# Kernel optimization log

Hardware: AMD Instinct MI355X
Metric: run time of the kernel (lower is better)

## Reference

```python
import jax, jax.numpy as jnp
import numpy as np

N = 100000      # nodes
E = 3200000     # edges (avg degree 32)
F_IN = 512      # input features
H = 16          # hidden (module default)
C = 40          # classes


def _linear_params(key, fan_in, fan_out):
    # torch.nn.Linear default init: U(-1/sqrt(fan_in), 1/sqrt(fan_in))
    k1, k2 = jax.random.split(key)
    lim = 1.0 / np.sqrt(fan_in)
    W = jax.random.uniform(k1, (fan_in, fan_out), jnp.float32, -lim, lim)
    b = jax.random.uniform(k2, (fan_out,), jnp.float32, -lim, lim)
    return W, b


def setup_inputs() -> dict:
    key = jax.random.key(0)
    ks = jax.random.split(key, 8)
    x = jax.random.normal(ks[0], (N, F_IN), jnp.float32)
    edge_index = jax.random.randint(ks[1], (2, E), 0, N, dtype=jnp.int64)
    edge_weight = jax.random.uniform(ks[2], (E,), jnp.float32)
    W_first, b_first = _linear_params(ks[3], F_IN, H)
    W_conv1, b_conv1 = _linear_params(ks[4], H, H)
    W_conv2, b_conv2 = _linear_params(ks[5], H, H)
    W_out, b_out = _linear_params(ks[6], H, C)
    return {
        "x": x, "edge_index": edge_index, "edge_weight": edge_weight,
        "W_first": W_first, "b_first": b_first,
        "W_conv1": W_conv1, "b_conv1": b_conv1,
        "W_conv2": W_conv2, "b_conv2": b_conv2,
        "W_out": W_out, "b_out": b_out,
    }


def _gcn_conv(x, W, b, row, col, ew):
    # PyG GCNConv: h = x @ W; out_i = sum_{(j->i)} norm_e * h_j + b
    # norm_e = deg^-1/2[row] * w_e * deg^-1/2[col], deg from target (col) index,
    # with self-loops (weight 1) already appended to row/col/ew.
    n = x.shape[0]
    deg = jax.ops.segment_sum(ew, col, num_segments=n)
    dinv = jnp.where(deg > 0, jax.lax.rsqrt(deg), 0.0)
    norm = dinv[row] * ew * dinv[col]
    h = x @ W
    out = jax.ops.segment_sum(h[row] * norm[:, None], col, num_segments=n)
    return out + b


def reference(x, edge_index, edge_weight, W_first, b_first,
              W_conv1, b_conv1, W_conv2, b_conv2, W_out, b_out):
    n = x.shape[0]
    # add self-loops once (shared by all conv layers)
    loop = jnp.arange(n, dtype=edge_index.dtype)
    row = jnp.concatenate([edge_index[0], loop])
    col = jnp.concatenate([edge_index[1], loop])
    ew = jnp.concatenate([edge_weight, jnp.ones((n,), edge_weight.dtype)])

    h = jax.nn.relu(x @ W_first + b_first)
    # dropout: eval mode -> identity
    h = jax.nn.relu(_gcn_conv(h, W_conv1, b_conv1, row, col, ew))
    h = jax.nn.relu(_gcn_conv(h, W_conv2, b_conv2, row, col, ew))
    # dropout: eval mode -> identity
    logits = h @ W_out + b_out
    return jax.nn.log_softmax(logits, axis=-1)
```

## Files before the change

kernel.cpp:

```cpp
#include <hip/hip_runtime.h>
#include <hip/hip_bf16.h>
#include <math.h>

#define F_IN 512
#define H 16
#define BSH 7
#define BNODES (1 << BSH)
#define SSH 12
#define EPT 64
#define CAP 5376
#define SEG 4096
#define SL 33


__global__ __launch_bounds__(256) void hist_kernel(const int* __restrict__ col,
                                                   int* __restrict__ bcnt, int E, int NBUCK) {
    extern __shared__ int hs[];
    const int t = threadIdx.x;
    for (int i = t; i < NBUCK; i += 256) hs[i] = 0;
    __syncthreads();
    long long e0 = (long long)blockIdx.x * (256 * EPT) + t;
#pragma unroll 4
    for (int k = 0; k < EPT; ++k) {
        long long e = e0 + (long long)k * 256;
        if (e < E) atomicAdd(&hs[col[e] >> BSH], 1);
    }
    __syncthreads();
    for (int i = t; i < NBUCK; i += 256) {
        int h = hs[i];
        if (h > 0) atomicAdd(&bcnt[i], h);
    }
}

__global__ void bscan_kernel(const int* __restrict__ bcnt, int* __restrict__ bbase,
                             int* __restrict__ sbase, int* __restrict__ rowptr,
                             int NBUCK, int nsup, int E, int N) {
    __shared__ int sm[1024];
    int t = threadIdx.x;
    int v = (t < NBUCK) ? bcnt[t] : 0;
    sm[t] = v;
    __syncthreads();
    for (int o = 1; o < 1024; o <<= 1) {
        int u = (t >= o) ? sm[t - o] : 0;
        __syncthreads();
        sm[t] += u;
        __syncthreads();
    }
    if (t < NBUCK) bbase[t] = sm[t] - v;
    if (t == 0) { bbase[NBUCK] = E; rowptr[N] = E; }
    __syncthreads();
    if (t < nsup) {
        int bk = t << (SSH - BSH);
        sbase[t] = (bk < NBUCK) ? (sm[bk] - bcnt[bk]) : E;
    }
    if (t == nsup) sbase[nsup] = E;
}


__global__ __launch_bounds__(256) void scat1_kernel(const int* __restrict__ row,
                                                    const int* __restrict__ col,
                                                    const float* __restrict__ ew,
                                                    const int* __restrict__ sbase,
                                                    int* __restrict__ sfill,
                                                    int2* __restrict__ ptmp, int E, int nsup) {
    __shared__ int2 stg[SEG];
    __shared__ unsigned char sup[SEG];
    __shared__ int cnt[32], base[32];
    const int t = threadIdx.x;
    const int e0 = blockIdx.x * SEG;
    int m = E - e0; if (m > SEG) m = SEG;
    if (t < 32) cnt[t] = 0;
    __syncthreads();
    for (int i = t; i < m; i += 256) {
        int e = e0 + i;
        int c = col[e];
        int s = c >> SSH;
        sup[i] = (unsigned char)s;
        atomicAdd(&cnt[s], 1);
        stg[i] = make_int2(row[e] | ((c & ((1 << SSH) - 1)) << 17), __float_as_int(ew[e]));
    }
    __syncthreads();
    if (t < nsup) {
        int h = cnt[t];
        base[t] = h ? atomicAdd(&sfill[t], h) : 0;
        cnt[t] = 0;
    }
    __syncthreads();
    for (int i = t; i < m; i += 256) {
        int s = sup[i];
        int rk = atomicAdd(&cnt[s], 1);
        ptmp[sbase[s] + base[s] + rk] = stg[i];
    }
}


__global__ __launch_bounds__(256) void scat2_kernel(const int* __restrict__ sbase,
                                                    const int* __restrict__ bbase,
                                                    int* __restrict__ ffill,
                                                    const int2* __restrict__ ptmp,
                                                    int2* __restrict__ packed, int NBUCK) {
    __shared__ int2 stg[SEG];
    __shared__ int cnt[32], base[32];
    const int t = threadIdx.x;
    const int s  = blockIdx.x / SL;
    const int sl = blockIdx.x % SL;
    const int ss = sbase[s];
    const int len = sbase[s + 1] - ss;
    const int lo = ss + (int)((long long)len * sl / SL);
    const int hi = ss + (int)((long long)len * (sl + 1) / SL);
    int m = hi - lo; if (m > SEG) m = SEG;
    if (t < 32) cnt[t] = 0;
    __syncthreads();
    for (int i = t; i < m; i += 256) {
        int2 p = ptmp[lo + i];
        stg[i] = p;
        int bk5 = ((unsigned)p.x >> (17 + BSH)) & 31;
        atomicAdd(&cnt[bk5], 1);
    }
    __syncthreads();
    if (t < 32) {
        int bk = (s << 5) + t;
        int h = cnt[t];
        base[t] = (h && bk < NBUCK) ? atomicAdd(&ffill[bk], h) : 0;
        cnt[t] = 0;
    }
    __syncthreads();
    for (int i = t; i < m; i += 256) {
        int2 p = stg[i];
        int bk5 = ((unsigned)p.x >> (17 + BSH)) & 31;
        int rk = atomicAdd(&cnt[bk5], 1);
        int bk = (s << 5) + bk5;
        packed[bbase[bk] + base[bk5] + rk] = make_int2(p.x & 0xFFFFFF, p.y);
    }
}

__global__ __launch_bounds__(256) void pass2_kernel(const int* __restrict__ bbase,
                                                    int2* __restrict__ packed,
                                                    int* __restrict__ rowptr,
                                                    float* __restrict__ dinv, int N) {
    __shared__ int2  edg[CAP];
    __shared__ int   ncnt[BNODES], nsc[BNODES], nfill[BNODES];
    __shared__ float dsum[BNODES];
    const int t = threadIdx.x;
    const int b = blockIdx.x;
    const int s = bbase[b];
    int cnt = bbase[b + 1] - s;
    if (cnt > CAP) cnt = CAP;

    for (int i = t; i < cnt; i += 256) edg[i] = packed[s + i];
    if (t < BNODES) { ncnt[t] = 0; nfill[t] = 0; dsum[t] = 0.f; }
    __syncthreads();

    for (int i = t; i < cnt; i += 256) {
        int lc = (edg[i].x >> 17) & (BNODES - 1);
        atomicAdd(&ncnt[lc], 1);
        atomicAdd(&dsum[lc], __int_as_float(edg[i].y));
    }
    __syncthreads();
    if (t < BNODES) nsc[t] = ncnt[t];
    __syncthreads();
    for (int o = 1; o < BNODES; o <<= 1) {
        int v = (t < BNODES && t >= o) ? nsc[t - o] : 0;
        __syncthreads();
        if (t < BNODES) nsc[t] += v;
        __syncthreads();
    }
    if (t < BNODES) {
        int n = b * BNODES + t;
        if (n < N) {
            rowptr[n] = s + nsc[t] - ncnt[t];
            dinv[n]   = rsqrtf(1.0f + dsum[t]);
        }
    }
    __syncthreads();
    for (int i = t; i < cnt; i += 256) {
        int lc = (edg[i].x >> 17) & (BNODES - 1);
        int rk = atomicAdd(&nfill[lc], 1);
        packed[s + nsc[lc] - ncnt[lc] + rk] = make_int2(edg[i].x & 0x1FFFF, edg[i].y);
    }
}


#define L1_ROWS 8
#define XS_CH 36
#define XS_ROW (16 * XS_CH)

__global__ __launch_bounds__(256) void l1_kernel(const float* __restrict__ x,
                                                 const float* __restrict__ W,
                                                 const float* __restrict__ b,
                                                 float* __restrict__ h0, int N) {
    __shared__ float xs[L1_ROWS][XS_ROW];
    __shared__ float part[L1_ROWS][256];
    const int t  = threadIdx.x;
    const int o  = t & 15;
    const int fg = t >> 4;

    float Wreg[32];
#pragma unroll
    for (int j = 0; j < 32; ++j) Wreg[j] = W[(fg * 32 + j) * H + o];
    const float bias = b[o];

    const int nbatch = (N + L1_ROWS - 1) / L1_ROWS;
    for (int batch = blockIdx.x; batch < nbatch; batch += gridDim.x) {
        const int row0 = batch * L1_ROWS;
#pragma unroll
        for (int bq = 0; bq < 4; ++bq) {
            int L  = bq * 256 + t;
            int rl = L >> 7;
            int f4 = L & 127;
            int r  = row0 + rl;
            float4 v = make_float4(0.f, 0.f, 0.f, 0.f);
            if (r < N) v = *(const float4*)&x[(size_t)r * F_IN + f4 * 4];
            int fgs = f4 >> 3, j4 = f4 & 7;
            *(float4*)&xs[rl][fgs * XS_CH + j4 * 4] = v;
        }
        __syncthreads();

        float acc[L1_ROWS];
#pragma unroll
        for (int r = 0; r < L1_ROWS; ++r) acc[r] = 0.f;
#pragma unroll
        for (int j4 = 0; j4 < 8; ++j4) {
#pragma unroll
            for (int r = 0; r < L1_ROWS; ++r) {
                float4 xv = *(const float4*)&xs[r][fg * XS_CH + j4 * 4];
                acc[r] = fmaf(xv.x, Wreg[j4 * 4 + 0], acc[r]);
                acc[r] = fmaf(xv.y, Wreg[j4 * 4 + 1], acc[r]);
                acc[r] = fmaf(xv.z, Wreg[j4 * 4 + 2], acc[r]);
                acc[r] = fmaf(xv.w, Wreg[j4 * 4 + 3], acc[r]);
            }
        }
#pragma unroll
        for (int r = 0; r < L1_ROWS; ++r) part[r][fg * 16 + o] = acc[r];
        __syncthreads();

        if (t < 128) {
            int r = t >> 4, oo = t & 15;
            float s = 0.f;
#pragma unroll
            for (int g = 0; g < 16; ++g) s += part[r][g * 16 + oo];
            s = fmaxf(s + bias, 0.f);
            int rr = row0 + r;
            if (rr < N) h0[(size_t)rr * H + oo] = s;
        }
        __syncthreads();
    }
}


__global__ __launch_bounds__(256) void mm16_kernel(const float* __restrict__ hin,
                                                   const float* __restrict__ W,
                                                   const float* __restrict__ dinv,
                                                   float* __restrict__ hWs, int N) {
    __shared__ float Wl[H * H];
    if (threadIdx.x < H * H) Wl[threadIdx.x] = W[threadIdx.x];
    __syncthreads();
    int n = blockIdx.x * 256 + threadIdx.x;
    if (n >= N) return;
    float hv[H];
#pragma unroll
    for (int k4 = 0; k4 < 4; ++k4) {
        float4 v = *(const float4*)&hin[(size_t)n * H + k4 * 4];
        hv[k4 * 4 + 0] = v.x; hv[k4 * 4 + 1] = v.y;
        hv[k4 * 4 + 2] = v.z; hv[k4 * 4 + 3] = v.w;
    }
    float acc[H];
#pragma unroll
    for (int c = 0; c < H; ++c) acc[c] = 0.f;
#pragma unroll
    for (int k = 0; k < H; ++k) {
#pragma unroll
        for (int c = 0; c < H; ++c) acc[c] = fmaf(hv[k], Wl[k * H + c], acc[c]);
    }
    float di = dinv[n];
#pragma unroll
    for (int c4 = 0; c4 < 4; ++c4) {
        float4 a = make_float4(di * acc[c4 * 4], di * acc[c4 * 4 + 1],
                               di * acc[c4 * 4 + 2], di * acc[c4 * 4 + 3]);
        *(float4*)&hWs[(size_t)n * H + c4 * 4] = a;
    }
}


__global__ __launch_bounds__(256) void gather_kernel(const int* __restrict__ rowptr,
                                                     const int2* __restrict__ packed,
                                                     const float* __restrict__ hWs,
                                                     const float* __restrict__ dinv,
                                                     const float* __restrict__ b,
                                                     float* __restrict__ out, int N) {
    int t = blockIdx.x * 256 + threadIdx.x;
    int n = t >> 4, f = t & 15;
    if (n >= N) return;
    int s = rowptr[n], e = rowptr[n + 1];
    float acc = hWs[(size_t)n * H + f];
    int i = s;
    for (; i + 2 <= e; i += 2) {
        int2 p0 = packed[i], p1 = packed[i + 1];
        float h0 = hWs[(size_t)p0.x * H + f];
        float h1 = hWs[(size_t)p1.x * H + f];
        acc = fmaf(__int_as_float(p0.y), h0, acc);
        acc = fmaf(__int_as_float(p1.y), h1, acc);
    }
    if (i < e) {
        int2 p = packed[i];
        acc = fmaf(__int_as_float(p.y), hWs[(size_t)p.x * H + f], acc);
    }
    out[(size_t)n * H + f] = fmaxf(fmaf(dinv[n], acc, b[f]), 0.f);
}


__global__ __launch_bounds__(256) void out_kernel(const float* __restrict__ h,
                                                  const float* __restrict__ W,
                                                  const float* __restrict__ b,
                                                  float* __restrict__ out, int N, int C) {
    extern __shared__ float sm[];
    float* Wl = sm;
    float* bl = sm + H * C;
    for (int i = threadIdx.x; i < H * C; i += 256) Wl[i] = W[i];
    if (threadIdx.x < C) bl[threadIdx.x] = b[threadIdx.x];
    __syncthreads();
    int n = blockIdx.x * 256 + threadIdx.x;
    if (n >= N) return;
    float hv[H];
#pragma unroll
    for (int k4 = 0; k4 < 4; ++k4) {
        float4 v = *(const float4*)&h[(size_t)n * H + k4 * 4];
        hv[k4 * 4 + 0] = v.x; hv[k4 * 4 + 1] = v.y;
        hv[k4 * 4 + 2] = v.z; hv[k4 * 4 + 3] = v.w;
    }
    float acc[40];
    for (int c = 0; c < C; ++c) acc[c] = bl[c];
    for (int k = 0; k < H; ++k) {
        float xk = hv[k];
        for (int c = 0; c < C; ++c) acc[c] = fmaf(xk, Wl[k * C + c], acc[c]);
    }
    float m = -1e30f;
    for (int c = 0; c < C; ++c) m = fmaxf(m, acc[c]);
    float s = 0.f;
    for (int c = 0; c < C; ++c) s += __expf(acc[c] - m);
    float lse = m + __logf(s);
    for (int c = 0; c < C; ++c) acc[c] -= lse;
    for (int c4 = 0; c4 < C / 4; ++c4) {
        float4 v = make_float4(acc[c4 * 4], acc[c4 * 4 + 1], acc[c4 * 4 + 2], acc[c4 * 4 + 3]);
        *(float4*)&out[(size_t)n * C + c4 * 4] = v;
    }
}


extern "C" void kernel_launch(void* const* d_in, const int* in_sizes, int n_in,
                              void* d_out, int out_size, void* d_ws, size_t ws_size,
                              hipStream_t stream) {
    const float* x       = (const float*)d_in[0];
    const int*   ei      = (const int*)d_in[1];
    const float* ew      = (const float*)d_in[2];
    const float* W_first = (const float*)d_in[3];
    const float* b_first = (const float*)d_in[4];
    const float* W_c1    = (const float*)d_in[5];
    const float* b_c1    = (const float*)d_in[6];
    const float* W_c2    = (const float*)d_in[7];
    const float* b_c2    = (const float*)d_in[8];
    const float* W_o     = (const float*)d_in[9];
    const float* b_o     = (const float*)d_in[10];

    const int N = in_sizes[0] / F_IN;
    const int E = in_sizes[2];
    const int C = in_sizes[10];
    const int NBUCK = (N + BNODES - 1) >> BSH;
    const int NSUP  = ((N - 1) >> SSH) + 1;
    const int HB    = (E + 256 * EPT - 1) / (256 * EPT);
    const int SB    = (E + SEG - 1) / SEG;

    const int* row = ei;
    const int* col = ei + E;

    char* wsb = (char*)d_ws;
    int*   bcnt   = (int*)wsb;                  wsb += (size_t)NBUCK * 4;
    int*   sfill  = (int*)wsb;                  wsb += (size_t)32 * 4;
    int*   ffill  = (int*)wsb;                  wsb += (size_t)NBUCK * 4;
    int*   bbase  = (int*)wsb;                  wsb += (size_t)(NBUCK + 1) * 4;
    int*   sbase  = (int*)wsb;                  wsb += (size_t)(NSUP + 1) * 4;
    int*   rowptr = (int*)wsb;                  wsb += (size_t)(N + 1) * 4;
    float* dinv   = (float*)wsb;                wsb += (size_t)N * 4;
    int2*  packed = (int2*)wsb;                 wsb += (size_t)E * 8;
    int2*  ptmp   = (int2*)wsb;                 wsb += (size_t)E * 8;
    float* bufA   = (float*)ptmp;
    float* bufB   = (float*)d_out;

    hipMemsetAsync(bcnt, 0, (size_t)(NBUCK * 2 + 32) * 4, stream);

    hist_kernel<<<HB, 256, NBUCK * 4, stream>>>(col, bcnt, E, NBUCK);
    bscan_kernel<<<1, 1024, 0, stream>>>(bcnt, bbase, sbase, rowptr, NBUCK, NSUP, E, N);
    scat1_kernel<<<SB, 256, 0, stream>>>(row, col, ew, sbase, sfill, ptmp, E, NSUP);
    scat2_kernel<<<NSUP * SL, 256, 0, stream>>>(sbase, bbase, ffill, ptmp, packed, NBUCK);
    pass2_kernel<<<NBUCK, 256, 0, stream>>>(bbase, packed, rowptr, dinv, N);

    l1_kernel<<<1024, 256, 0, stream>>>(x, W_first, b_first, bufA, N);

    mm16_kernel<<<(N + 255) / 256, 256, 0, stream>>>(bufA, W_c1, dinv, bufB, N);
    gather_kernel<<<(N * 16 + 255) / 256, 256, 0, stream>>>(rowptr, packed, bufB, dinv, b_c1, bufA, N);

    mm16_kernel<<<(N + 255) / 256, 256, 0, stream>>>(bufA, W_c2, dinv, bufB, N);
    gather_kernel<<<(N * 16 + 255) / 256, 256, 0, stream>>>(rowptr, packed, bufB, dinv, b_c2, bufA, N);

    size_t smem = (size_t)(H * C + C) * sizeof(float);
    out_kernel<<<(N + 255) / 256, 256, smem, stream>>>(bufA, W_o, b_o, (float*)d_out, N, C);
}
```

Measured before the change: 686.0 us.

## Aggregate before transform and fuse conv matmuls and output softmax into gather

Reorders each GCN layer to aggregate first, then apply the 16x16 weight, using (A·X)W = A·(XW). The small matmul now runs inside the gather kernel through wave shuffles, and the dinv prescale moves into the producing kernel. The last conv also computes the output linear layer and log-softmax in the same kernel. This removes the two mm16 launches, the separate out kernel and their intermediate round trips to memory, at the cost of shuffle overhead and a hardcoded class count of 40.

```diff
diff --git a/kernel.cpp b/kernel.cpp
--- a/kernel.cpp
+++ b/kernel.cpp
@@ -4,6 +4,7 @@
 
 #define F_IN 512
 #define H 16
+#define COUT 40
 #define BSH 7
 #define BNODES (1 << BSH)
 #define SSH 12
@@ -188,7 +189,8 @@
 __global__ __launch_bounds__(256) void l1_kernel(const float* __restrict__ x,
                                                  const float* __restrict__ W,
                                                  const float* __restrict__ b,
-                                                 float* __restrict__ h0, int N) {
+                                                 const float* __restrict__ dinv,
+                                                 float* __restrict__ g0, int N) {
     __shared__ float xs[L1_ROWS][XS_ROW];
     __shared__ float part[L1_ROWS][256];
     const int t  = threadIdx.x;
@@ -241,108 +243,90 @@
             for (int g = 0; g < 16; ++g) s += part[r][g * 16 + oo];
             s = fmaxf(s + bias, 0.f);
             int rr = row0 + r;
-            if (rr < N) h0[(size_t)rr * H + oo] = s;
-        }
-        __syncthreads();
-    }
-}
-
-
-__global__ __launch_bounds__(256) void mm16_kernel(const float* __restrict__ hin,
-                                                   const float* __restrict__ W,
+            if (rr < N) g0[(size_t)rr * H + oo] = s * dinv[rr];
+        }
+        __syncthreads();
+    }
+}
+
+
+template<bool LAST>
+__global__ __launch_bounds__(256) void conv_kernel(const int* __restrict__ rowptr,
+                                                   const int2* __restrict__ packed,
+                                                   const float* __restrict__ g_in,
                                                    const float* __restrict__ dinv,
-                                                   float* __restrict__ hWs, int N) {
-    __shared__ float Wl[H * H];
-    if (threadIdx.x < H * H) Wl[threadIdx.x] = W[threadIdx.x];
-    __syncthreads();
-    int n = blockIdx.x * 256 + threadIdx.x;
+                                                   const float* __restrict__ Wc,
+                                                   const float* __restrict__ bc,
+                                                   const float* __restrict__ Wo,
+                                                   const float* __restrict__ bo,
+                                                   float* __restrict__ out, int N) {
+    __shared__ float Wcs[H * H];
+    __shared__ float bcs[H];
+    __shared__ float Wos[H * 48];
+    __shared__ float bos[48];
+    const int tt = threadIdx.x;
+    if (tt < H * H) Wcs[tt] = Wc[tt];
+    if (tt < H) bcs[tt] = bc[tt];
+    if (LAST) {
+        for (int i = tt; i < H * 48; i += 256) {
+            int f = i / 48, c = i % 48;
+            Wos[i] = (c < COUT) ? Wo[f * COUT + c] : 0.f;
+        }
+        if (tt < 48) bos[tt] = (tt < COUT) ? bo[tt] : 0.f;
+    }
+    __syncthreads();
+
+    int t = blockIdx.x * 256 + tt;
+    int n = t >> 4, o = t & 15;
     if (n >= N) return;
-    float hv[H];
-#pragma unroll
-    for (int k4 = 0; k4 < 4; ++k4) {
-        float4 v = *(const float4*)&hin[(size_t)n * H + k4 * 4];
-        hv[k4 * 4 + 0] = v.x; hv[k4 * 4 + 1] = v.y;
-        hv[k4 * 4 + 2] = v.z; hv[k4 * 4 + 3] = v.w;
-    }
-    float acc[H];
-#pragma unroll
-    for (int c = 0; c < H; ++c) acc[c] = 0.f;
-#pragma unroll
-    for (int k = 0; k < H; ++k) {
-#pragma unroll
-        for (int c = 0; c < H; ++c) acc[c] = fmaf(hv[k], Wl[k * H + c], acc[c]);
-    }
-    float di = dinv[n];
-#pragma unroll
-    for (int c4 = 0; c4 < 4; ++c4) {
-        float4 a = make_float4(di * acc[c4 * 4], di * acc[c4 * 4 + 1],
-                               di * acc[c4 * 4 + 2], di * acc[c4 * 4 + 3]);
-        *(float4*)&hWs[(size_t)n * H + c4 * 4] = a;
-    }
-}
-
-
-__global__ __launch_bounds__(256) void gather_kernel(const int* __restrict__ rowptr,
-                                                     const int2* __restrict__ packed,
-                                                     const float* __restrict__ hWs,
-                                                     const float* __restrict__ dinv,
-                                                     const float* __restrict__ b,
-                                                     float* __restrict__ out, int N) {
-    int t = blockIdx.x * 256 + threadIdx.x;
-    int n = t >> 4, f = t & 15;
-    if (n >= N) return;
+
     int s = rowptr[n], e = rowptr[n + 1];
-    float acc = hWs[(size_t)n * H + f];
+    float acc = g_in[(size_t)n * H + o];
     int i = s;
     for (; i + 2 <= e; i += 2) {
         int2 p0 = packed[i], p1 = packed[i + 1];
-        float h0 = hWs[(size_t)p0.x * H + f];
-        float h1 = hWs[(size_t)p1.x * H + f];
-        acc = fmaf(__int_as_float(p0.y), h0, acc);
-        acc = fmaf(__int_as_float(p1.y), h1, acc);
+        float ga = g_in[(size_t)p0.x * H + o];
+        float gb = g_in[(size_t)p1.x * H + o];
+        acc = fmaf(__int_as_float(p0.y), ga, acc);
+        acc = fmaf(__int_as_float(p1.y), gb, acc);
     }
     if (i < e) {
         int2 p = packed[i];
-        acc = fmaf(__int_as_float(p.y), hWs[(size_t)p.x * H + f], acc);
-    }
-    out[(size_t)n * H + f] = fmaxf(fmaf(dinv[n], acc, b[f]), 0.f);
-}
-
-
-__global__ __launch_bounds__(256) void out_kernel(const float* __restrict__ h,
-                                                  const float* __restrict__ W,
-                                                  const float* __restrict__ b,
-                                                  float* __restrict__ out, int N, int C) {
-    extern __shared__ float sm[];
-    float* Wl = sm;
-    float* bl = sm + H * C;
-    for (int i = threadIdx.x; i < H * C; i += 256) Wl[i] = W[i];
-    if (threadIdx.x < C) bl[threadIdx.x] = b[threadIdx.x];
-    __syncthreads();
-    int n = blockIdx.x * 256 + threadIdx.x;
-    if (n >= N) return;
-    float hv[H];
-#pragma unroll
-    for (int k4 = 0; k4 < 4; ++k4) {
-        float4 v = *(const float4*)&h[(size_t)n * H + k4 * 4];
-        hv[k4 * 4 + 0] = v.x; hv[k4 * 4 + 1] = v.y;
-        hv[k4 * 4 + 2] = v.z; hv[k4 * 4 + 3] = v.w;
-    }
-    float acc[40];
-    for (int c = 0; c < C; ++c) acc[c] = bl[c];
-    for (int k = 0; k < H; ++k) {
-        float xk = hv[k];
-        for (int c = 0; c < C; ++c) acc[c] = fmaf(xk, Wl[k * C + c], acc[c]);
-    }
-    float m = -1e30f;
-    for (int c = 0; c < C; ++c) m = fmaxf(m, acc[c]);
-    float s = 0.f;
-    for (int c = 0; c < C; ++c) s += __expf(acc[c] - m);
-    float lse = m + __logf(s);
-    for (int c = 0; c < C; ++c) acc[c] -= lse;
-    for (int c4 = 0; c4 < C / 4; ++c4) {
-        float4 v = make_float4(acc[c4 * 4], acc[c4 * 4 + 1], acc[c4 * 4 + 2], acc[c4 * 4 + 3]);
-        *(float4*)&out[(size_t)n * C + c4 * 4] = v;
+        acc = fmaf(__int_as_float(p.y), g_in[(size_t)p.x * H + o], acc);
+    }
+    const float di = dinv[n];
+    const float y = di * acc;
+
+    float h = bcs[o];
+#pragma unroll
+    for (int f = 0; f < H; ++f) {
+        float yf = __shfl(y, f, 16);
+        h = fmaf(yf, Wcs[f * H + o], h);
+    }
+    h = fmaxf(h, 0.f);
+
+    if (!LAST) {
+        out[(size_t)n * H + o] = di * h;
+    } else {
+        float l0 = bos[o], l1 = bos[o + 16], l2 = bos[o + 32];
+#pragma unroll
+        for (int f = 0; f < H; ++f) {
+            float hf = __shfl(h, f, 16);
+            l0 = fmaf(hf, Wos[f * 48 + o], l0);
+            l1 = fmaf(hf, Wos[f * 48 + o + 16], l1);
+            l2 = fmaf(hf, Wos[f * 48 + o + 32], l2);
+        }
+        float m = fmaxf(l0, l1);
+        if (o < 8) m = fmaxf(m, l2);
+#pragma unroll
+        for (int d = 1; d < 16; d <<= 1) m = fmaxf(m, __shfl_xor(m, d, 16));
+        float sx = __expf(l0 - m) + __expf(l1 - m) + ((o < 8) ? __expf(l2 - m) : 0.f);
+#pragma unroll
+        for (int d = 1; d < 16; d <<= 1) sx += __shfl_xor(sx, d, 16);
+        float lse = m + __logf(sx);
+        out[(size_t)n * COUT + o]      = l0 - lse;
+        out[(size_t)n * COUT + o + 16] = l1 - lse;
+        if (o < 8) out[(size_t)n * COUT + o + 32] = l2 - lse;
     }
 }
 
@@ -364,7 +348,6 @@
 
     const int N = in_sizes[0] / F_IN;
     const int E = in_sizes[2];
-    const int C = in_sizes[10];
     const int NBUCK = (N + BNODES - 1) >> BSH;
     const int NSUP  = ((N - 1) >> SSH) + 1;
     const int HB    = (E + 256 * EPT - 1) / (256 * EPT);
@@ -383,8 +366,8 @@
     float* dinv   = (float*)wsb;                wsb += (size_t)N * 4;
     int2*  packed = (int2*)wsb;                 wsb += (size_t)E * 8;
     int2*  ptmp   = (int2*)wsb;                 wsb += (size_t)E * 8;
-    float* bufA   = (float*)ptmp;
-    float* bufB   = (float*)d_out;
+    float* g0     = (float*)ptmp;
+    float* g1     = (float*)ptmp + (size_t)N * H;
 
     hipMemsetAsync(bcnt, 0, (size_t)(NBUCK * 2 + 32) * 4, stream);
 
@@ -394,14 +377,11 @@
     scat2_kernel<<<NSUP * SL, 256, 0, stream>>>(sbase, bbase, ffill, ptmp, packed, NBUCK);
     pass2_kernel<<<NBUCK, 256, 0, stream>>>(bbase, packed, rowptr, dinv, N);
 
-    l1_kernel<<<1024, 256, 0, stream>>>(x, W_first, b_first, bufA, N);
-
-    mm16_kernel<<<(N + 255) / 256, 256, 0, stream>>>(bufA, W_c1, dinv, bufB, N);
-    gather_kernel<<<(N * 16 + 255) / 256, 256, 0, stream>>>(rowptr, packed, bufB, dinv, b_c1, bufA, N);
-
-    mm16_kernel<<<(N + 255) / 256, 256, 0, stream>>>(bufA, W_c2, dinv, bufB, N);
-    gather_kernel<<<(N * 16 + 255) / 256, 256, 0, stream>>>(rowptr, packed, bufB, dinv, b_c2, bufA, N);
-
-    size_t smem = (size_t)(H * C + C) * sizeof(float);
-    out_kernel<<<(N + 255) / 256, 256, smem, stream>>>(bufA, W_o, b_o, (float*)d_out, N, C);
-}
+    l1_kernel<<<1024, 256, 0, stream>>>(x, W_first, b_first, dinv, g0, N);
+
+    conv_kernel<false><<<(N * 16 + 255) / 256, 256, 0, stream>>>(
+        rowptr, packed, g0, dinv, W_c1, b_c1, nullptr, nullptr, g1, N);
+
+    conv_kernel<true><<<(N * 16 + 255) / 256, 256, 0, stream>>>(
+        rowptr, packed, g1, dinv, W_c2, b_c2, W_o, b_o, (float*)d_out, N);
+}
```

Result: faster. 590.4 us (-13.9%).
